# Performance work log

Measured on AMD Instinct MI355X. Metric: run time of the kernel, lower is better.

## Reference

```python
import jax, jax.numpy as jnp
import numpy as np

D_MODEL = 1024
N_HEAD = 16
B, T = 4, 1024
MAX_REL = 32  # max_relative_positions


def setup_inputs() -> dict:
    key = jax.random.key(0)
    ks = jax.random.split(key, 12)
    s = 0.02
    inp = {
        "x": jax.random.normal(ks[0], (B, T, D_MODEL), jnp.float32),
        "mask": jnp.tril(jnp.ones((T, T), dtype=bool)),  # causal mask, 1 = keep
        "Wq": jax.random.normal(ks[1], (D_MODEL, D_MODEL), jnp.float32) * s,
        "bq": jax.random.normal(ks[2], (D_MODEL,), jnp.float32) * s,
        "Wk": jax.random.normal(ks[3], (D_MODEL, D_MODEL), jnp.float32) * s,
        "bk": jax.random.normal(ks[4], (D_MODEL,), jnp.float32) * s,
        "Wv": jax.random.normal(ks[5], (D_MODEL, D_MODEL), jnp.float32) * s,
        "bv": jax.random.normal(ks[6], (D_MODEL,), jnp.float32) * s,
        "Wo": jax.random.normal(ks[7], (D_MODEL, D_MODEL), jnp.float32) * s,
        "bo": jax.random.normal(ks[8], (D_MODEL,), jnp.float32) * s,
        "rel_bias": jax.random.normal(ks[9], (2 * MAX_REL - 1, N_HEAD), jnp.float32) * s,
        "n_head": N_HEAD,
    }
    return inp


def reference(x, mask, Wq, bq, Wk, bk, Wv, bv, Wo, bo, rel_bias, n_head):
    Bx, Tx, C = x.shape
    Dh = C // n_head
    scale = Dh ** (-0.5)
    # projections: torch Linear is x @ W.T + b
    Q = (x @ Wq.T + bq).reshape(Bx, Tx, n_head, Dh)
    K = (x @ Wk.T + bk).reshape(Bx, Tx, n_head, Dh)
    V = (x @ Wv.T + bv).reshape(Bx, Tx, n_head, Dh)
    # scores: [B, H, T, T]
    scores = jnp.einsum("bqhd,bkhd->bhqk", Q, K) * scale
    # T5-style clipped relative-position bias
    pos = jnp.arange(Tx)
    rel = pos[None, :] - pos[:, None]                     # k_pos - q_pos, [T, T]
    buckets = jnp.clip(rel, -(MAX_REL - 1), MAX_REL - 1) + (MAX_REL - 1)
    bias = rel_bias[buckets]                              # [T, T, H]
    scores = scores + jnp.transpose(bias, (2, 0, 1))[None]
    # original applies masked_fill(-inf) then masked_fill(0): net effect = 0
    scores = jnp.where(mask, scores, 0.0)
    w = jax.nn.relu(scores) + 1e-6
    w = jnp.where(mask, w, 0.0)
    w = w / (jnp.sum(w, axis=-1, keepdims=True) + 1e-6)
    out = jnp.einsum("bhqk,bkhd->bqhd", w, V).reshape(Bx, Tx, C)
    return out @ Wo.T + bo
```

## Files before the change

### kernel.cpp

```cpp
#include <hip/hip_runtime.h>


typedef __attribute__((ext_vector_type(8))) __bf16 bf16x8;
typedef __attribute__((ext_vector_type(4))) __bf16 bf16x4;
typedef __attribute__((ext_vector_type(4))) float f32x4;
typedef unsigned short u16;

__device__ __forceinline__ u16 f2bf(float f) {
  unsigned u = __float_as_uint(f);
  u += 0x7FFFu + ((u >> 16) & 1u);
  return (u16)(u >> 16);
}
__device__ __forceinline__ float bf2f(u16 b) {
  return __uint_as_float(((unsigned)b) << 16);
}
__device__ __forceinline__ void gl_lds16(const void* g, void* l) {
  __builtin_amdgcn_global_load_lds((__attribute__((address_space(1))) void*)g,
                                   (__attribute__((address_space(3))) void*)l,
                                   16, 0, 0);
}

__global__ __launch_bounds__(256) void cast_all_kernel(
    const float* __restrict__ x,  const float* __restrict__ wq,
    const float* __restrict__ wk, const float* __restrict__ wv,
    const float* __restrict__ wo,
    u16* __restrict__ xb, u16* __restrict__ wqb, u16* __restrict__ wkb,
    u16* __restrict__ wvb, u16* __restrict__ wob) {
  long i4 = (long)blockIdx.x * 256 + threadIdx.x;
  const float* src; u16* dst; long rel;
  if (i4 < 1048576) { src = x; dst = xb; rel = i4; }
  else {
    long j = i4 - 1048576;
    int w = (int)(j >> 18);
    rel = j & 262143;
    src = (w == 0) ? wq : (w == 1) ? wk : (w == 2) ? wv : wo;
    dst = (w == 0) ? wqb : (w == 1) ? wkb : (w == 2) ? wvb : wob;
  }
  float4 v = ((const float4*)src)[rel];
  ushort4 o;
  o.x = f2bf(v.x); o.y = f2bf(v.y); o.z = f2bf(v.z); o.w = f2bf(v.w);
  ((ushort4*)dst)[rel] = o;
}

template <bool STORE_BF16>
__device__ __forceinline__ void gemm_body(
    const u16* __restrict__ A, const u16* __restrict__ B,
    const float* __restrict__ bias, bool rowbias,
    void* __restrict__ Cout, int ldc, int m0, int n0) {
  constexpr int K = 1024;
  constexpr int NT = K / 64;
  __shared__ __align__(16) u16 As[2][128 * 64];
  __shared__ __align__(16) u16 Bs[2][128 * 64];

  const int t = threadIdx.x;
  const int lane = t & 63;
  const int wv = t >> 6;
  const int quad = lane >> 4;
  const int l15 = lane & 15;
  const int wr = wv >> 1, wc = wv & 1;
  const int sw0 = (quad ^ (l15 & 7)) * 8;
  const int sw1 = ((4 + quad) ^ (l15 & 7)) * 8;

  const f32x4 vzero = {0.f, 0.f, 0.f, 0.f};
  f32x4 acc[4][4];
#pragma unroll
  for (int i = 0; i < 4; ++i)
#pragma unroll
    for (int j = 0; j < 4; ++j) acc[i][j] = vzero;

  auto stage = [&](int kt, int bufi) {
#pragma unroll
    for (int p = 0; p < 4; ++p) {
      int idx = t + p * 256;
      int row = idx >> 3, seg = idx & 7;
      int sseg = seg ^ (row & 7);
      gl_lds16(&A[(long)(m0 + row) * K + kt * 64 + sseg * 8], &As[bufi][idx * 8]);
      gl_lds16(&B[(long)(n0 + row) * K + kt * 64 + sseg * 8], &Bs[bufi][idx * 8]);
    }
  };

  stage(0, 0);
  for (int kt = 0; kt < NT; ++kt) {
    const int bufi = kt & 1;
    if (kt + 1 < NT) {
      stage(kt + 1, bufi ^ 1);
      asm volatile("s_waitcnt vmcnt(8)" ::: "memory");
    } else {
      asm volatile("s_waitcnt vmcnt(0)" ::: "memory");
    }
    asm volatile("s_barrier" ::: "memory");
#pragma unroll
    for (int ks = 0; ks < 64; ks += 32) {
      const int sw = ks ? sw1 : sw0;
      bf16x8 af[4], bfg[4];
#pragma unroll
      for (int i = 0; i < 4; ++i)
        af[i] = *(const bf16x8*)&As[bufi][(wr * 64 + i * 16 + l15) * 64 + sw];
#pragma unroll
      for (int j = 0; j < 4; ++j)
        bfg[j] = *(const bf16x8*)&Bs[bufi][(wc * 64 + j * 16 + l15) * 64 + sw];
#pragma unroll
      for (int i = 0; i < 4; ++i)
#pragma unroll
        for (int j = 0; j < 4; ++j)
          acc[i][j] = __builtin_amdgcn_mfma_f32_16x16x32_bf16(af[i], bfg[j], acc[i][j], 0, 0, 0);
    }
    asm volatile("s_barrier" ::: "memory");
  }

  float cb[4];
  if (!rowbias) {
#pragma unroll
    for (int j = 0; j < 4; ++j) cb[j] = bias[n0 + wc * 64 + j * 16 + l15];
  }

#pragma unroll
  for (int i = 0; i < 4; ++i) {
#pragma unroll
    for (int r = 0; r < 4; ++r) {
      int row = m0 + wr * 64 + i * 16 + quad * 4 + r;
      long base = (long)row * ldc + n0 + wc * 64;
      float rb_ = rowbias ? bias[row] : 0.f;
#pragma unroll
      for (int j = 0; j < 4; ++j) {
        float v = acc[i][j][r] + (rowbias ? rb_ : cb[j]);
        if (STORE_BF16) ((u16*)Cout)[base + j * 16 + l15] = f2bf(v);
        else            ((float*)Cout)[base + j * 16 + l15] = v;
      }
    }
  }
}

template <bool STORE_BF16>
__device__ __forceinline__ void gemm256_body(
    const u16* __restrict__ A, const u16* __restrict__ B,
    const float* __restrict__ bias, bool rowbias,
    void* __restrict__ Cout, int ldc, int m0, int n0) {
  constexpr int K = 1024;
  constexpr int NT = K / 64;
  __shared__ __align__(16) u16 As[2][2][256 * 32];
  __shared__ __align__(16) u16 Bs[2][2][256 * 32];

  const int t = threadIdx.x;
  const int lane = t & 63;
  const int wv = t >> 6;
  const int wr = wv >> 2;
  const int wc = wv & 3;
  const int quad = lane >> 4;
  const int l15 = lane & 15;

  const int rA = wr * 128 + l15;
  const int rB = wc * 64 + l15;
  const int baseA = rA * 32 + ((quad ^ ((rA >> 1) & 3)) * 8);
  const int baseB = rB * 32 + ((quad ^ ((rB >> 1) & 3)) * 8);

  const int srow = t >> 2;
  const int sg = (t & 3) ^ ((t >> 3) & 3);
  const long sA = (long)(m0 + srow) * K + sg * 8;
  const long sB = (long)(n0 + srow) * K + sg * 8;

  auto stA = [&](int T_, int kh, int bf_) {
    const u16* s = A + sA + T_ * 64 + kh * 32;
    u16* d = &As[bf_][kh][t * 8];
    gl_lds16(s, d);
    gl_lds16(s + (long)128 * K, d + 4096);
  };
  auto stB = [&](int T_, int kh, int bf_) {
    const u16* s = B + sB + T_ * 64 + kh * 32;
    u16* d = &Bs[bf_][kh][t * 8];
    gl_lds16(s, d);
    gl_lds16(s + (long)128 * K, d + 4096);
  };

  const f32x4 vzero = {0.f, 0.f, 0.f, 0.f};
  f32x4 acc[8][4];
#pragma unroll
  for (int i = 0; i < 8; ++i)
#pragma unroll
    for (int j = 0; j < 4; ++j) acc[i][j] = vzero;

  stA(0, 0, 0); stB(0, 0, 0);
  stA(0, 1, 0); stB(0, 1, 0);
  stA(1, 0, 1); stB(1, 0, 1);
  asm volatile("s_waitcnt vmcnt(4)" ::: "memory");
  asm volatile("s_barrier" ::: "memory");

  for (int T = 0; T < NT; ++T) {
    const int c = T & 1;
    const u16* Ac = &As[c][0][0];
    const u16* Bc = &Bs[c][0][0];
    bf16x8 af[4], bfr[4];

#pragma unroll
    for (int j = 0; j < 4; ++j) bfr[j] = *(const bf16x8*)&Bc[baseB + j * 512];
#pragma unroll
    for (int i = 0; i < 4; ++i) af[i] = *(const bf16x8*)&Ac[baseA + i * 512];
    if (T + 1 < NT) stA(T + 1, 1, c ^ 1);
    asm volatile("s_barrier" ::: "memory");
    __builtin_amdgcn_s_setprio(1);
#pragma unroll
    for (int i = 0; i < 4; ++i)
#pragma unroll
      for (int j = 0; j < 4; ++j)
        acc[i][j] = __builtin_amdgcn_mfma_f32_16x16x32_bf16(af[i], bfr[j], acc[i][j], 0, 0, 0);
    __builtin_amdgcn_s_setprio(0);
    asm volatile("s_barrier" ::: "memory");

#pragma unroll
    for (int i = 0; i < 4; ++i) af[i] = *(const bf16x8*)&Ac[baseA + 2048 + i * 512];
    if (T + 1 < NT) stB(T + 1, 1, c ^ 1);
    asm volatile("s_barrier" ::: "memory");
    __builtin_amdgcn_s_setprio(1);
#pragma unroll
    for (int i = 0; i < 4; ++i)
#pragma unroll
      for (int j = 0; j < 4; ++j)
        acc[4 + i][j] = __builtin_amdgcn_mfma_f32_16x16x32_bf16(af[i], bfr[j], acc[4 + i][j], 0, 0, 0);
    __builtin_amdgcn_s_setprio(0);
    asm volatile("s_barrier" ::: "memory");

    if (T == NT - 1) {
      asm volatile("s_waitcnt vmcnt(0)" ::: "memory");
      asm volatile("s_barrier" ::: "memory");
    }
#pragma unroll
    for (int j = 0; j < 4; ++j) bfr[j] = *(const bf16x8*)&Bc[8192 + baseB + j * 512];
#pragma unroll
    for (int i = 0; i < 4; ++i) af[i] = *(const bf16x8*)&Ac[8192 + baseA + i * 512];
    if (T + 2 < NT) stA(T + 2, 0, c);
    asm volatile("s_barrier" ::: "memory");
    __builtin_amdgcn_s_setprio(1);
#pragma unroll
    for (int i = 0; i < 4; ++i)
#pragma unroll
      for (int j = 0; j < 4; ++j)
        acc[i][j] = __builtin_amdgcn_mfma_f32_16x16x32_bf16(af[i], bfr[j], acc[i][j], 0, 0, 0);
    __builtin_amdgcn_s_setprio(0);
    asm volatile("s_barrier" ::: "memory");

#pragma unroll
    for (int i = 0; i < 4; ++i) af[i] = *(const bf16x8*)&Ac[8192 + baseA + 2048 + i * 512];
    if (T + 2 < NT) stB(T + 2, 0, c);
    asm volatile("s_barrier" ::: "memory");
    __builtin_amdgcn_s_setprio(1);
#pragma unroll
    for (int i = 0; i < 4; ++i)
#pragma unroll
      for (int j = 0; j < 4; ++j)
        acc[4 + i][j] = __builtin_amdgcn_mfma_f32_16x16x32_bf16(af[i], bfr[j], acc[4 + i][j], 0, 0, 0);
    __builtin_amdgcn_s_setprio(0);
    asm volatile("s_waitcnt vmcnt(4)" ::: "memory");
    asm volatile("s_barrier" ::: "memory");
  }

  float cb[4];
  if (!rowbias) {
#pragma unroll
    for (int j = 0; j < 4; ++j) cb[j] = bias[n0 + wc * 64 + j * 16 + l15];
  }

#pragma unroll
  for (int mf = 0; mf < 8; ++mf) {
#pragma unroll
    for (int r = 0; r < 4; ++r) {
      int row = m0 + wr * 128 + mf * 16 + quad * 4 + r;
      long base = (long)row * ldc + n0 + wc * 64;
      float rb_ = rowbias ? bias[row] : 0.f;
#pragma unroll
      for (int j = 0; j < 4; ++j) {
        float v = acc[mf][j][r] + (rowbias ? rb_ : cb[j]);
        if (STORE_BF16) ((u16*)Cout)[base + j * 16 + l15] = f2bf(v);
        else            ((float*)Cout)[base + j * 16 + l15] = v;
      }
    }
  }
}

__global__ __launch_bounds__(512, 2) void gemm_qkv(
    const u16* __restrict__ xb, const u16* __restrict__ wqb,
    const u16* __restrict__ wkb, const u16* __restrict__ wvb,
    const float* __restrict__ bq, const float* __restrict__ bk,
    const float* __restrict__ bv,
    u16* __restrict__ Qb, u16* __restrict__ Kb, u16* __restrict__ Vtg) {
  const int bx = blockIdx.x;
  const int L = (bx & 7) * 24 + (bx >> 3);
  const u16 *AT, *BT;
  const float* bias;
  u16* C;
  int m0, n0, ldc;
  bool rowbias;
  if (L < 128) {
    int sel = L >> 6;
    int g = L & 63;
    m0 = (g >> 2) * 256; n0 = (g & 3) * 256;
    AT = xb; BT = sel ? wkb : wqb; bias = sel ? bk : bq;
    C = sel ? Kb : Qb; ldc = 1024; rowbias = false;
  } else {
    int g = L - 128;
    m0 = (g & 3) * 256; n0 = (g >> 2) * 256;
    AT = wvb; BT = xb; bias = bv;
    C = Vtg; ldc = 4096; rowbias = true;
  }
  gemm256_body<true>(AT, BT, bias, rowbias, C, ldc, m0, n0);
}

__global__ __launch_bounds__(256) void gemm_out(
    const u16* __restrict__ A, const u16* __restrict__ B,
    const float* __restrict__ bias, float* __restrict__ C) {
  gemm_body<false>(A, B, bias, false, C, 1024, blockIdx.x * 128, blockIdx.y * 128);
}

__global__ __launch_bounds__(512) void attn_strip(
    const u16* __restrict__ Qb,
    const u16* __restrict__ Kb,
    const u16* __restrict__ Vtg,
    const float* __restrict__ rel_bias,
    u16* __restrict__ att) {
  constexpr int WS = 68;
  __shared__ __align__(16) u16 Kt[2][64 * 64];
  __shared__ __align__(16) u16 Vt[2][64 * 64];
  __shared__ __align__(16) u16 Ws[8][16 * WS];
  __shared__ float biasl[64];

  const int bx = blockIdx.x;
  const int strip = 7 - (bx >> 6);
  const int bh = bx & 63;
  const int b = bh >> 4, h = bh & 15;
  const int q0 = strip * 128;
  const int cend = 2 * strip + 1;

  const int t = threadIdx.x;
  const int lane = t & 63;
  const int wv = t >> 6;
  const int quad = lane >> 4;
  const int l15 = lane & 15;

  if (t < 63) biasl[t] = rel_bias[t * 16 + h];
  const float b0c = rel_bias[h];

  const int srow = t >> 3;
  const int sseg = (t & 7) ^ (srow & 7);
  const u16* Ksrc = &Kb[(long)(b * 1024 + srow) * 1024 + h * 64 + sseg * 8];
  const u16* Vsrc = &Vtg[(long)(h * 64 + srow) * 4096 + b * 1024 + sseg * 8];

  auto stage = [&](int c, int bufi) {
    const int k0 = c * 64;
    gl_lds16(Ksrc + (long)k0 * 1024, &Kt[bufi][t * 8]);
    gl_lds16(Vsrc + k0,              &Vt[bufi][t * 8]);
  };

  const long qrow = (long)(b * 1024 + q0 + wv * 16 + l15) * 1024 + h * 64;
  bf16x8 qf0 = *(const bf16x8*)&Qb[qrow + quad * 8];
  bf16x8 qf1 = *(const bf16x8*)&Qb[qrow + 32 + quad * 8];

  const f32x4 vzero = {0.f, 0.f, 0.f, 0.f};
  f32x4 acc_o[4];
#pragma unroll
  for (int j = 0; j < 4; ++j) acc_o[j] = vzero;
  float denom = 0.f;
  const float scale = 0.125f;
  const int ql = q0 + wv * 16 + l15;
  const int sw0 = (quad ^ (l15 & 7)) * 8;
  const int sw1 = ((4 + quad) ^ (l15 & 7)) * 8;

  stage(0, 0);

  for (int c = 0; c <= cend; ++c) {
    const int buf = c & 1;
    const int k0 = c * 64;
    __syncthreads();
    if (c + 1 <= cend) stage(c + 1, buf ^ 1);

    const bool fast = (c <= 2 * strip - 2);
#pragma unroll
    for (int g = 0; g < 4; ++g) {
      const u16* kr = &Kt[buf][(g * 16 + l15) * 64];
      bf16x8 kf0 = *(const bf16x8*)&kr[sw0];
      bf16x8 kf1 = *(const bf16x8*)&kr[sw1];
      f32x4 sT = vzero;
      sT = __builtin_amdgcn_mfma_f32_16x16x32_bf16(kf0, qf0, sT, 0, 0, 0);
      sT = __builtin_amdgcn_mfma_f32_16x16x32_bf16(kf1, qf1, sT, 0, 0, 0);
      const int kgb = k0 + g * 16 + quad * 4;
      ushort4 wpk;
      if (fast) {
#pragma unroll
        for (int r = 0; r < 4; ++r) {
          float w = fmaxf(sT[r] * scale + b0c, 0.f) + 1e-6f;
          u16 wb = f2bf(w);
          denom += bf2f(wb);
          ((u16*)&wpk)[r] = wb;
        }
      } else {
#pragma unroll
        for (int r = 0; r < 4; ++r) {
          int kg = kgb + r;
          int dd = kg - ql;
          dd = dd < -31 ? -31 : (dd > 31 ? 31 : dd);
          float sv = sT[r] * scale + biasl[dd + 31];
          float w = (kg <= ql) ? (fmaxf(sv, 0.f) + 1e-6f) : 0.f;
          u16 wb = f2bf(w);
          denom += bf2f(wb);
          ((u16*)&wpk)[r] = wb;
        }
      }
      *(ushort4*)&Ws[wv][l15 * WS + g * 16 + quad * 4] = wpk;
    }
    asm volatile("s_waitcnt lgkmcnt(0)" ::: "memory");
#pragma unroll
    for (int ks = 0; ks < 64; ks += 32) {
      union { bf16x8 v8; bf16x4 v4[2]; } au;
      int wbase = l15 * WS + ks + quad * 8;
      au.v4[0] = *(const bf16x4*)&Ws[wv][wbase];
      au.v4[1] = *(const bf16x4*)&Ws[wv][wbase + 4];
      const int sv = ks ? sw1 : sw0;
#pragma unroll
      for (int j = 0; j < 4; ++j) {
        bf16x8 bvv = *(const bf16x8*)&Vt[buf][(j * 16 + l15) * 64 + sv];
        acc_o[j] = __builtin_amdgcn_mfma_f32_16x16x32_bf16(au.v8, bvv, acc_o[j], 0, 0, 0);
      }
    }
  }

  denom += __shfl_xor(denom, 16);
  denom += __shfl_xor(denom, 32);

  float invm = 1.f / (denom + 1e-6f);
  float inv[4];
#pragma unroll
  for (int r = 0; r < 4; ++r) inv[r] = __shfl(invm, quad * 4 + r);
#pragma unroll
  for (int j = 0; j < 4; ++j)
#pragma unroll
    for (int r = 0; r < 4; ++r) {
      int q = q0 + wv * 16 + quad * 4 + r;
      att[(long)(b * 1024 + q) * 1024 + h * 64 + j * 16 + l15] = f2bf(acc_o[j][r] * inv[r]);
    }
}

extern "C" void kernel_launch(void* const* d_in, const int* in_sizes, int n_in,
                              void* d_out, int out_size, void* d_ws, size_t ws_size,
                              hipStream_t stream) {
  const float* x  = (const float*)d_in[0];
  const float* Wq = (const float*)d_in[2];
  const float* bq = (const float*)d_in[3];
  const float* Wk = (const float*)d_in[4];
  const float* bk = (const float*)d_in[5];
  const float* Wv = (const float*)d_in[6];
  const float* bv = (const float*)d_in[7];
  const float* Wo = (const float*)d_in[8];
  const float* bo = (const float*)d_in[9];
  const float* rb = (const float*)d_in[10];

  char* ws = (char*)d_ws;
  u16* xb  = (u16*)(ws);
  u16* wqb = (u16*)(ws + (8l  << 20));
  u16* wkb = (u16*)(ws + (10l << 20));
  u16* wvb = (u16*)(ws + (12l << 20));
  u16* wob = (u16*)(ws + (14l << 20));
  u16* Qb  = (u16*)(ws + (16l << 20));
  u16* Kb  = (u16*)d_out;
  u16* Vtg = (u16*)((char*)d_out + (8l << 20));

  cast_all_kernel<<<8192, 256, 0, stream>>>(x, Wq, Wk, Wv, Wo, xb, wqb, wkb, wvb, wob);
  gemm_qkv<<<192, 512, 0, stream>>>(xb, wqb, wkb, wvb, bq, bk, bv, Qb, Kb, Vtg);
  attn_strip<<<512, 512, 0, stream>>>(Qb, Kb, Vtg, rb, Qb);
  gemm_out<<<dim3(32, 8), 256, 0, stream>>>(Qb, wob, bo, (float*)d_out);
}
```

Measured before the change: 183.8 us.

## Give each attention wave two query tiles and halve threads per block

The attention kernel drops from 512 to 256 threads per block, and each wave now handles 32 query rows as two 16-row groups. Each K and V fragment read from LDS is reused across both groups, and each thread stages two rows of K/V per chunk. The bf16 packing of the weights switches to the hardware v_cvt_pk_bf16_f32 instruction instead of manual rounding. This cuts LDS reads per MFMA, at the cost of more registers per thread and fewer waves available to hide latency.

After: 191.8 us. +4.3%, slower.

```diff
diff --git a/kernel.cpp b/kernel.cpp
--- a/kernel.cpp
+++ b/kernel.cpp
@@ -13,6 +13,11 @@
 }
 __device__ __forceinline__ float bf2f(u16 b) {
   return __uint_as_float(((unsigned)b) << 16);
+}
+__device__ __forceinline__ unsigned cvt_pk_bf16(float lo, float hi) {
+  unsigned r;
+  asm("v_cvt_pk_bf16_f32 %0, %1, %2" : "=v"(r) : "v"(lo), "v"(hi));
+  return r;
 }
 __device__ __forceinline__ void gl_lds16(const void* g, void* l) {
   __builtin_amdgcn_global_load_lds((__attribute__((address_space(1))) void*)g,
@@ -310,16 +315,16 @@
   gemm_body<false>(A, B, bias, false, C, 1024, blockIdx.x * 128, blockIdx.y * 128);
 }
 
-__global__ __launch_bounds__(512) void attn_strip(
+__global__ __launch_bounds__(256) void attn_strip(
     const u16* __restrict__ Qb,
     const u16* __restrict__ Kb,
     const u16* __restrict__ Vtg,
     const float* __restrict__ rel_bias,
     u16* __restrict__ att) {
-  constexpr int WS = 68;
+  constexpr int WS = 72;
   __shared__ __align__(16) u16 Kt[2][64 * 64];
   __shared__ __align__(16) u16 Vt[2][64 * 64];
-  __shared__ __align__(16) u16 Ws[8][16 * WS];
+  __shared__ __align__(16) u16 Ws[4][2][16 * WS];
   __shared__ float biasl[64];
 
   const int bx = blockIdx.x;
@@ -338,28 +343,40 @@
   if (t < 63) biasl[t] = rel_bias[t * 16 + h];
   const float b0c = rel_bias[h];
 
-  const int srow = t >> 3;
-  const int sseg = (t & 7) ^ (srow & 7);
-  const u16* Ksrc = &Kb[(long)(b * 1024 + srow) * 1024 + h * 64 + sseg * 8];
-  const u16* Vsrc = &Vtg[(long)(h * 64 + srow) * 4096 + b * 1024 + sseg * 8];
+  const int r0s = t >> 3;
+  const int s0s = (t & 7) ^ (r0s & 7);
+  const int r1s = r0s + 32;
+  const int s1s = (t & 7) ^ (r1s & 7);
+  const u16* Ksrc0 = &Kb[(long)(b * 1024 + r0s) * 1024 + h * 64 + s0s * 8];
+  const u16* Ksrc1 = &Kb[(long)(b * 1024 + r1s) * 1024 + h * 64 + s1s * 8];
+  const u16* Vsrc0 = &Vtg[(long)(h * 64 + r0s) * 4096 + b * 1024 + s0s * 8];
+  const u16* Vsrc1 = &Vtg[(long)(h * 64 + r1s) * 4096 + b * 1024 + s1s * 8];
 
   auto stage = [&](int c, int bufi) {
     const int k0 = c * 64;
-    gl_lds16(Ksrc + (long)k0 * 1024, &Kt[bufi][t * 8]);
-    gl_lds16(Vsrc + k0,              &Vt[bufi][t * 8]);
+    gl_lds16(Ksrc0 + (long)k0 * 1024, &Kt[bufi][t * 8]);
+    gl_lds16(Ksrc1 + (long)k0 * 1024, &Kt[bufi][t * 8 + 2048]);
+    gl_lds16(Vsrc0 + k0,              &Vt[bufi][t * 8]);
+    gl_lds16(Vsrc1 + k0,              &Vt[bufi][t * 8 + 2048]);
   };
 
-  const long qrow = (long)(b * 1024 + q0 + wv * 16 + l15) * 1024 + h * 64;
-  bf16x8 qf0 = *(const bf16x8*)&Qb[qrow + quad * 8];
-  bf16x8 qf1 = *(const bf16x8*)&Qb[qrow + 32 + quad * 8];
+  bf16x8 qf0[2], qf1[2];
+#pragma unroll
+  for (int gq = 0; gq < 2; ++gq) {
+    const long qrow = (long)(b * 1024 + q0 + wv * 32 + gq * 16 + l15) * 1024 + h * 64;
+    qf0[gq] = *(const bf16x8*)&Qb[qrow + quad * 8];
+    qf1[gq] = *(const bf16x8*)&Qb[qrow + 32 + quad * 8];
+  }
 
   const f32x4 vzero = {0.f, 0.f, 0.f, 0.f};
-  f32x4 acc_o[4];
-#pragma unroll
-  for (int j = 0; j < 4; ++j) acc_o[j] = vzero;
-  float denom = 0.f;
+  f32x4 acc_o[2][4];
+#pragma unroll
+  for (int gq = 0; gq < 2; ++gq)
+#pragma unroll
+    for (int j = 0; j < 4; ++j) acc_o[gq][j] = vzero;
+  float denom[2] = {0.f, 0.f};
   const float scale = 0.125f;
-  const int ql = q0 + wv * 16 + l15;
+  const int ql0 = q0 + wv * 32 + l15;
   const int sw0 = (quad ^ (l15 & 7)) * 8;
   const int sw1 = ((4 + quad) ^ (l15 & 7)) * 8;
 
@@ -377,64 +394,69 @@
       const u16* kr = &Kt[buf][(g * 16 + l15) * 64];
       bf16x8 kf0 = *(const bf16x8*)&kr[sw0];
       bf16x8 kf1 = *(const bf16x8*)&kr[sw1];
-      f32x4 sT = vzero;
-      sT = __builtin_amdgcn_mfma_f32_16x16x32_bf16(kf0, qf0, sT, 0, 0, 0);
-      sT = __builtin_amdgcn_mfma_f32_16x16x32_bf16(kf1, qf1, sT, 0, 0, 0);
       const int kgb = k0 + g * 16 + quad * 4;
-      ushort4 wpk;
-      if (fast) {
-#pragma unroll
-        for (int r = 0; r < 4; ++r) {
-          float w = fmaxf(sT[r] * scale + b0c, 0.f) + 1e-6f;
-          u16 wb = f2bf(w);
-          denom += bf2f(wb);
-          ((u16*)&wpk)[r] = wb;
+#pragma unroll
+      for (int gq = 0; gq < 2; ++gq) {
+        f32x4 sT = vzero;
+        sT = __builtin_amdgcn_mfma_f32_16x16x32_bf16(kf0, qf0[gq], sT, 0, 0, 0);
+        sT = __builtin_amdgcn_mfma_f32_16x16x32_bf16(kf1, qf1[gq], sT, 0, 0, 0);
+        float w[4];
+        if (fast) {
+#pragma unroll
+          for (int r = 0; r < 4; ++r)
+            w[r] = fmaxf(sT[r] * scale + b0c, 0.f) + 1e-6f;
+        } else {
+          const int ql = ql0 + gq * 16;
+#pragma unroll
+          for (int r = 0; r < 4; ++r) {
+            int kg = kgb + r;
+            int dd = kg - ql;
+            dd = dd < -31 ? -31 : (dd > 31 ? 31 : dd);
+            float sv = sT[r] * scale + biasl[dd + 31];
+            w[r] = (kg <= ql) ? (fmaxf(sv, 0.f) + 1e-6f) : 0.f;
+          }
         }
-      } else {
-#pragma unroll
-        for (int r = 0; r < 4; ++r) {
-          int kg = kgb + r;
-          int dd = kg - ql;
-          dd = dd < -31 ? -31 : (dd > 31 ? 31 : dd);
-          float sv = sT[r] * scale + biasl[dd + 31];
-          float w = (kg <= ql) ? (fmaxf(sv, 0.f) + 1e-6f) : 0.f;
-          u16 wb = f2bf(w);
-          denom += bf2f(wb);
-          ((u16*)&wpk)[r] = wb;
-        }
+        unsigned p0 = cvt_pk_bf16(w[0], w[1]);
+        unsigned p1 = cvt_pk_bf16(w[2], w[3]);
+        denom[gq] += __uint_as_float(p0 << 16) + __uint_as_float(p0 & 0xFFFF0000u) +
+                     __uint_as_float(p1 << 16) + __uint_as_float(p1 & 0xFFFF0000u);
+        uint2 pk; pk.x = p0; pk.y = p1;
+        *(uint2*)&Ws[wv][gq][l15 * WS + g * 16 + quad * 4] = pk;
       }
-      *(ushort4*)&Ws[wv][l15 * WS + g * 16 + quad * 4] = wpk;
     }
     asm volatile("s_waitcnt lgkmcnt(0)" ::: "memory");
 #pragma unroll
     for (int ks = 0; ks < 64; ks += 32) {
-      union { bf16x8 v8; bf16x4 v4[2]; } au;
-      int wbase = l15 * WS + ks + quad * 8;
-      au.v4[0] = *(const bf16x4*)&Ws[wv][wbase];
-      au.v4[1] = *(const bf16x4*)&Ws[wv][wbase + 4];
+      bf16x8 pa0 = *(const bf16x8*)&Ws[wv][0][l15 * WS + ks + quad * 8];
+      bf16x8 pa1 = *(const bf16x8*)&Ws[wv][1][l15 * WS + ks + quad * 8];
       const int sv = ks ? sw1 : sw0;
 #pragma unroll
       for (int j = 0; j < 4; ++j) {
         bf16x8 bvv = *(const bf16x8*)&Vt[buf][(j * 16 + l15) * 64 + sv];
-        acc_o[j] = __builtin_amdgcn_mfma_f32_16x16x32_bf16(au.v8, bvv, acc_o[j], 0, 0, 0);
+        acc_o[0][j] = __builtin_amdgcn_mfma_f32_16x16x32_bf16(pa0, bvv, acc_o[0][j], 0, 0, 0);
+        acc_o[1][j] = __builtin_amdgcn_mfma_f32_16x16x32_bf16(pa1, bvv, acc_o[1][j], 0, 0, 0);
       }
     }
   }
 
-  denom += __shfl_xor(denom, 16);
-  denom += __shfl_xor(denom, 32);
-
-  float invm = 1.f / (denom + 1e-6f);
-  float inv[4];
-#pragma unroll
-  for (int r = 0; r < 4; ++r) inv[r] = __shfl(invm, quad * 4 + r);
-#pragma unroll
-  for (int j = 0; j < 4; ++j)
-#pragma unroll
-    for (int r = 0; r < 4; ++r) {
-      int q = q0 + wv * 16 + quad * 4 + r;
-      att[(long)(b * 1024 + q) * 1024 + h * 64 + j * 16 + l15] = f2bf(acc_o[j][r] * inv[r]);
-    }
+#pragma unroll
+  for (int gq = 0; gq < 2; ++gq) {
+    float dn = denom[gq];
+    dn += __shfl_xor(dn, 16);
+    dn += __shfl_xor(dn, 32);
+    float invm = 1.f / (dn + 1e-6f);
+    float inv[4];
+#pragma unroll
+    for (int r = 0; r < 4; ++r) inv[r] = __shfl(invm, quad * 4 + r);
+#pragma unroll
+    for (int j = 0; j < 4; ++j)
+#pragma unroll
+      for (int r = 0; r < 4; ++r) {
+        int q = q0 + wv * 32 + gq * 16 + quad * 4 + r;
+        att[(long)(b * 1024 + q) * 1024 + h * 64 + j * 16 + l15] =
+            f2bf(acc_o[gq][j][r] * inv[r]);
+      }
+  }
 }
 
 extern "C" void kernel_launch(void* const* d_in, const int* in_sizes, int n_in,
@@ -462,7 +484,7 @@
   u16* Vtg = (u16*)((char*)d_out + (8l << 20));
 
   cast_all_kernel<<<8192, 256, 0, stream>>>(x, Wq, Wk, Wv, Wo, xb, wqb, wkb, wvb, wob);
-  gemm_qkv<<<192, 512, 0, stream>>>(xb, wqb, wkb, wvb, bq, bk, bv, Qb, Kb, Vtg);
-  attn_strip<<<512, 512, 0, stream>>>(Qb, Kb, Vtg, rb, Qb);
+  gemm_qkv<<<768 / 4, 512, 0, stream>>>(xb, wqb, wkb, wvb, bq, bk, bv, Qb, Kb, Vtg);
+  attn_strip<<<512, 256, 0, stream>>>(Qb, Kb, Vtg, rb, Qb);
   gemm_out<<<dim3(32, 8), 256, 0, stream>>>(Qb, wob, bo, (float*)d_out);
 }
```
